# Kernel optimization log

Measured on AMD Instinct MI355X. Metric: run time of the kernel, lower is better.

## Reference

```python
import jax, jax.numpy as jnp
import numpy as np

EMBED_DIM = 1024
HEAD_DIM = 64
B, T = 4, 4096


def setup_inputs() -> dict:
    key = jax.random.key(0)
    kx, kq, kk, kv = jax.random.split(key, 4)
    x = jax.random.normal(kx, (B, T, EMBED_DIM), dtype=jnp.float32)
    # nn.Linear weights, stored transposed as (in, out) for x @ W
    s = 1.0 / np.sqrt(EMBED_DIM)
    Wq = jax.random.normal(kq, (EMBED_DIM, HEAD_DIM), dtype=jnp.float32) * s
    Wk = jax.random.normal(kk, (EMBED_DIM, HEAD_DIM), dtype=jnp.float32) * s
    Wv = jax.random.normal(kv, (EMBED_DIM, HEAD_DIM), dtype=jnp.float32) * s
    return {"x": x, "Wq": Wq, "Wk": Wk, "Wv": Wv}


def reference(x, Wq, Wk, Wv):
    Bc, Tc, C = x.shape
    Q = x @ Wq  # [B, T, H]
    K = x @ Wk
    V = x @ Wv
    # NOTE: original scales by embedding_dim C, not head_dim
    scores = jnp.einsum('bqh,bkh->bqk', Q, K) / jnp.sqrt(jnp.float32(C))
    causal = jnp.tril(jnp.ones((Tc, Tc), dtype=bool))
    scores = jnp.where(causal, scores, -jnp.inf)
    attn = jax.nn.softmax(scores, axis=-1)
    return jnp.einsum('bqk,bkh->bqh', attn, V)
```

## Files before the change

### kernel.cpp

```cpp
#include <hip/hip_runtime.h>
#include <hip/hip_bf16.h>
#include <math.h>

typedef __attribute__((ext_vector_type(8))) short bf16x8;
typedef __attribute__((ext_vector_type(4))) float f32x4;

#define MFMA16 __builtin_amdgcn_mfma_f32_16x16x32_bf16

static constexpr int TSEQ = 4096;
static constexpr int EMB = 1024;
static constexpr int HD = 64;

__device__ __forceinline__ unsigned short f2bf(float f) {
    unsigned u = __builtin_bit_cast(unsigned, f);
    u += 0x7fffu + ((u >> 16) & 1u);
    return (unsigned short)(u >> 16);
}
__device__ __forceinline__ int pk2bf(float a, float b) {
    return (int)((unsigned)f2bf(a) | ((unsigned)f2bf(b) << 16));
}

union frag_u { int i[4]; bf16x8 v; };

__global__ void prep_w(const float* __restrict__ Wq, const float* __restrict__ Wk,
                       const float* __restrict__ Wv, unsigned short* __restrict__ Wp) {
    int id = blockIdx.x * 256 + threadIdx.x;
    int wsel = id >> 16;
    int t = id & 65535;
    int k = t >> 6, n0 = t & 63;
    const float* W = (wsel == 0) ? Wq : (wsel == 1) ? Wk : Wv;
    float v = W[t];
    if (wsel == 0) v *= 0.03125f;
    int n = wsel * 64 + n0;
    Wp[(k >> 5) * 6144 + n * 32 + (k & 31)] = f2bf(v);
}

__global__ __launch_bounds__(256, 4) void proj_kernel(const float* __restrict__ X,
        const unsigned short* __restrict__ Wp, unsigned short* __restrict__ Qp,
        unsigned short* __restrict__ Kp, unsigned short* __restrict__ Vp) {
    const int lane = threadIdx.x & 63, wave = threadIdx.x >> 6;
    const int col = lane & 15, quad = lane >> 4;
    const int row0 = blockIdx.x * 16;

    f32x4 acc[3];
#pragma unroll
    for (int j = 0; j < 3; j++) acc[j] = (f32x4)(0.0f);

    const float* xr = X + (size_t)(row0 + col) * EMB + quad * 8;
    const char* wB = (const char*)Wp + wave * 1024 + col * 64 + quad * 16;

    float4 xa[3][2];
    bf16x8 wf[3][3];
#pragma unroll
    for (int p = 0; p < 3; p++) {
        const float* xp = xr + p * 32;
        xa[p][0] = *(const float4*)(xp);
        xa[p][1] = *(const float4*)(xp + 4);
        const char* wp = wB + (size_t)p * 12288;
#pragma unroll
        for (int j = 0; j < 3; j++) wf[p][j] = *(const bf16x8*)(wp + j * 4096);
    }

#pragma unroll
    for (int kc = 0; kc < 32; kc++) {
        const int s = kc % 3;
        frag_u A;
        A.i[0] = pk2bf(xa[s][0].x, xa[s][0].y);
        A.i[1] = pk2bf(xa[s][0].z, xa[s][0].w);
        A.i[2] = pk2bf(xa[s][1].x, xa[s][1].y);
        A.i[3] = pk2bf(xa[s][1].z, xa[s][1].w);
#pragma unroll
        for (int j = 0; j < 3; j++)
            acc[j] = MFMA16(A.v, wf[s][j], acc[j], 0, 0, 0);
        if (kc + 3 < 32) {
            const float* xp = xr + (kc + 3) * 32;
            xa[s][0] = *(const float4*)(xp);
            xa[s][1] = *(const float4*)(xp + 4);
            const char* wp = wB + (size_t)(kc + 3) * 12288;
#pragma unroll
            for (int j = 0; j < 3; j++) wf[s][j] = *(const bf16x8*)(wp + j * 4096);
        }
    }

    const int tile = blockIdx.x;
    const int c = tile >> 1, j2 = tile & 1;
#pragma unroll
    for (int r = 0; r < 4; r++)
        Qp[tile * 1024 + (wave >> 1) * 512 + (quad * 4 + r) * 32 +
           ((wave & 1) * 2 + (col >> 3)) * 8 + (col & 7)] = f2bf(acc[0][r]);
#pragma unroll
    for (int r = 0; r < 4; r++)
        Kp[(tile * 2 + (wave >> 1)) * 512 + (quad * 4 + r) * 32 +
           ((wave & 1) * 2 + (col >> 3)) * 8 + (col & 7)] = f2bf(acc[1][r]);
    {
        ushort4 pk;
        pk.x = f2bf(acc[2][0]); pk.y = f2bf(acc[2][1]);
        pk.z = f2bf(acc[2][2]); pk.w = f2bf(acc[2][3]);
        *(ushort4*)&Vp[c * 2048 + wave * 512 + col * 32 + j2 * 16 + quad * 4] = pk;
    }
}

__global__ __launch_bounds__(512, 4) void attn_kernel(const unsigned short* __restrict__ Qp,
        const unsigned short* __restrict__ Kp, const unsigned short* __restrict__ Vp,
        float* __restrict__ Out) {
    __shared__ float cmb[4][2][64][20];
    __shared__ unsigned short plds[8][2][640];
    const int lane = threadIdx.x & 63, wave = threadIdx.x >> 6;
    const int col = lane & 15, quad = lane >> 4;
    const int batch = blockIdx.x & 3;
    const int ti = 127 - (blockIdx.x >> 2);
    const int q0 = ti * 32;
    const size_t bT = (size_t)batch * TSEQ;
    const int fragoff = col * 64 + quad * 16;

    const char* QpB = (const char*)Qp;
    const char* KpB = (const char*)Kp;
    const char* VpB = (const char*)Vp;
    const int gt = (int)((bT + q0) >> 4);
    const int c0 = (int)(bT >> 5);

    bf16x8 aq[2][2];
#pragma unroll
    for (int m = 0; m < 2; m++)
#pragma unroll
        for (int h = 0; h < 2; h++)
            aq[m][h] = *(const bf16x8*)(QpB + (size_t)((gt + m) * 2 + h) * 1024 + fragoff);

    f32x4 o[2][4];
    f32x4 lsum[2];
#pragma unroll
    for (int m = 0; m < 2; m++) {
        lsum[m] = (f32x4)(0.0f);
#pragma unroll
        for (int t = 0; t < 4; t++) o[m][t] = (f32x4)(0.0f);
    }

    for (int c = wave; c <= ti; c += 8) {
        const char* kb = KpB + (size_t)(c0 + c) * 4096;
        const char* vb = VpB + (size_t)(c0 + c) * 4096;
        bf16x8 bk[2][2], bv[4];
#pragma unroll
        for (int j = 0; j < 2; j++)
#pragma unroll
            for (int h = 0; h < 2; h++)
                bk[j][h] = *(const bf16x8*)(kb + j * 2048 + h * 1024 + fragoff);
#pragma unroll
        for (int t = 0; t < 4; t++)
            bv[t] = *(const bf16x8*)(vb + t * 1024 + fragoff);

        f32x4 s[2][2];
#pragma unroll
        for (int m = 0; m < 2; m++)
#pragma unroll
            for (int j = 0; j < 2; j++) {
                f32x4 a = MFMA16(aq[m][0], bk[j][0], (f32x4)(0.0f), 0, 0, 0);
                s[m][j] = MFMA16(aq[m][1], bk[j][1], a, 0, 0, 0);
            }
        const bool diag = (c == ti);
#pragma unroll
        for (int m = 0; m < 2; m++)
#pragma unroll
            for (int j = 0; j < 2; j++)
#pragma unroll
                for (int r = 0; r < 4; r++) {
                    float v = s[m][j][r];
                    if (diag && (j * 16 + col > m * 16 + quad * 4 + r)) v = -INFINITY;
                    const float p = __expf(v);
                    lsum[m][r] += p;
                    plds[wave][m][(quad * 4 + r) * 40 + j * 16 + col] =
                        (unsigned short)(__builtin_bit_cast(unsigned, p) >> 16);
                }
        bf16x8 pa[2];
#pragma unroll
        for (int m = 0; m < 2; m++)
            pa[m] = *(const bf16x8*)(&plds[wave][m][col * 40 + quad * 8]);
#pragma unroll
        for (int m = 0; m < 2; m++)
#pragma unroll
            for (int t = 0; t < 4; t++)
                o[m][t] = MFMA16(pa[m], bv[t], o[m][t], 0, 0, 0);
    }

    auto wr = [&](int s) {
#pragma unroll
        for (int m = 0; m < 2; m++) {
#pragma unroll
            for (int t = 0; t < 4; t++)
                *(f32x4*)&cmb[s][m][lane][t * 4] = o[m][t];
            *(f32x4*)&cmb[s][m][lane][16] = lsum[m];
        }
    };
    auto rd = [&](int s) {
#pragma unroll
        for (int m = 0; m < 2; m++) {
#pragma unroll
            for (int t = 0; t < 4; t++)
                o[m][t] += *(const f32x4*)&cmb[s][m][lane][t * 4];
            lsum[m] += *(const f32x4*)&cmb[s][m][lane][16];
        }
    };
    if (wave >= 4) wr(wave - 4);
    __syncthreads();
    if (wave < 4) rd(wave);
    __syncthreads();
    if (wave == 2 || wave == 3) wr(wave);
    __syncthreads();
    if (wave < 2) rd(wave + 2);
    __syncthreads();
    if (wave == 1) wr(1);
    __syncthreads();
    if (wave == 0) {
        rd(1);
#pragma unroll
        for (int off = 1; off < 16; off <<= 1)
#pragma unroll
            for (int m = 0; m < 2; m++)
#pragma unroll
                for (int r = 0; r < 4; r++)
                    lsum[m][r] += __shfl_xor(lsum[m][r], off, 64);
#pragma unroll
        for (int m = 0; m < 2; m++)
#pragma unroll
            for (int r = 0; r < 4; r++) {
                const float inv = 1.0f / lsum[m][r];
                const size_t orow = (bT + q0 + m * 16 + quad * 4 + r) * HD;
#pragma unroll
                for (int t = 0; t < 4; t++)
                    Out[orow + t * 16 + col] = o[m][t][r] * inv;
            }
    }
}

extern "C" void kernel_launch(void* const* d_in, const int* in_sizes, int n_in,
                              void* d_out, int out_size, void* d_ws, size_t ws_size,
                              hipStream_t stream) {
    const float* x  = (const float*)d_in[0];
    const float* Wq = (const float*)d_in[1];
    const float* Wk = (const float*)d_in[2];
    const float* Wv = (const float*)d_in[3];
    float* out = (float*)d_out;

    char* w = (char*)d_ws;
    unsigned short* Wp = (unsigned short*)(w);
    unsigned short* Qp = (unsigned short*)(w + (512 << 10));
    unsigned short* Kp = (unsigned short*)(w + (512 << 10) + (2 << 20));
    unsigned short* Vp = (unsigned short*)(w + (512 << 10) + (4 << 20));

    hipLaunchKernelGGL(prep_w, dim3(768), dim3(256), 0, stream, Wq, Wk, Wv, Wp);
    hipLaunchKernelGGL(proj_kernel, dim3(1024), dim3(256), 0, stream, x, Wp, Qp, Kp, Vp);
    hipLaunchKernelGGL(attn_kernel, dim3(512), dim3(512), 0, stream, Qp, Kp, Vp, out);
}
```

Baseline: 166.7 us.

## Stage projection weights and X tiles through double-buffered LDS with warp specialization

The projection kernel now handles 32 rows per 512-thread block. Half the waves stream weight slabs into LDS via global_load_lds, and the other half convert X to bf16 into LDS, both double-buffered. All waves then read MFMA fragments from LDS, so each weight slab is fetched once per 32 rows instead of once per 16, halving weight traffic. The cost is a __syncthreads every k-step and serialized producer/consumer roles, which may limit latency hiding compared with the register prefetch it replaces.

New measurement: 147.2 us. 11.7% less time.

```diff
diff --git a/kernel.cpp b/kernel.cpp
--- a/kernel.cpp
+++ b/kernel.cpp
@@ -16,11 +16,12 @@
     u += 0x7fffu + ((u >> 16) & 1u);
     return (unsigned short)(u >> 16);
 }
-__device__ __forceinline__ int pk2bf(float a, float b) {
-    return (int)((unsigned)f2bf(a) | ((unsigned)f2bf(b) << 16));
-}
-
-union frag_u { int i[4]; bf16x8 v; };
+
+__device__ __forceinline__ void gll16(const void* g, void* l) {
+    __builtin_amdgcn_global_load_lds(
+        (const __attribute__((address_space(1))) void*)g,
+        (__attribute__((address_space(3))) void*)l, 16, 0, 0);
+}
 
 __global__ void prep_w(const float* __restrict__ Wq, const float* __restrict__ Wk,
                        const float* __restrict__ Wv, unsigned short* __restrict__ Wp) {
@@ -35,68 +36,83 @@
     Wp[(k >> 5) * 6144 + n * 32 + (k & 31)] = f2bf(v);
 }
 
-__global__ __launch_bounds__(256, 4) void proj_kernel(const float* __restrict__ X,
+__global__ __launch_bounds__(512, 4) void proj_kernel(const float* __restrict__ X,
         const unsigned short* __restrict__ Wp, unsigned short* __restrict__ Qp,
         unsigned short* __restrict__ Kp, unsigned short* __restrict__ Vp) {
-    const int lane = threadIdx.x & 63, wave = threadIdx.x >> 6;
+    __shared__ unsigned short wlds[2][6144];
+    __shared__ unsigned short xlds[2][1024];
+
+    const int tid = threadIdx.x;
+    const int lane = tid & 63, wave = tid >> 6;
     const int col = lane & 15, quad = lane >> 4;
-    const int row0 = blockIdx.x * 16;
+    const int mw = wave >> 2, nw = wave & 3;
+    const int row0 = blockIdx.x * 32;
 
     f32x4 acc[3];
 #pragma unroll
     for (int j = 0; j < 3; j++) acc[j] = (f32x4)(0.0f);
 
-    const float* xr = X + (size_t)(row0 + col) * EMB + quad * 8;
-    const char* wB = (const char*)Wp + wave * 1024 + col * 64 + quad * 16;
-
-    float4 xa[3][2];
-    bf16x8 wf[3][3];
-#pragma unroll
-    for (int p = 0; p < 3; p++) {
-        const float* xp = xr + p * 32;
-        xa[p][0] = *(const float4*)(xp);
-        xa[p][1] = *(const float4*)(xp + 4);
-        const char* wp = wB + (size_t)p * 12288;
-#pragma unroll
-        for (int j = 0; j < 3; j++) wf[p][j] = *(const bf16x8*)(wp + j * 4096);
-    }
-
-#pragma unroll
+    const char* wsrc = (const char*)Wp + lane * 16;
+    auto stageW = [&](int slab, int b) {
+        const char* s = wsrc + (size_t)slab * 12288;
+        char* d = (char*)&wlds[b][0];
+        gll16(s + nw * 1024,       d + nw * 1024);
+        gll16(s + (4 + nw) * 1024, d + (4 + nw) * 1024);
+        gll16(s + (8 + nw) * 1024, d + (8 + nw) * 1024);
+    };
+    const int u = tid - 256;
+    const int xrow = u >> 3, xseg = u & 7;
+    const float* xsrc = X + (size_t)(row0 + xrow) * EMB + xseg * 4;
+    const int xdst = (xrow >> 4) * 1024 + (xseg >> 1) * 256 + (xrow & 15) * 16 + (xseg & 1) * 8;
+
+    float4 xg = (float4)(0.0f);
+    if (mw == 1) {
+        float4 v = *(const float4*)(xsrc);
+        ushort4 p; p.x = f2bf(v.x); p.y = f2bf(v.y); p.z = f2bf(v.z); p.w = f2bf(v.w);
+        *(ushort4*)((char*)&xlds[0][0] + xdst) = p;
+        xg = *(const float4*)(xsrc + 32);
+    } else {
+        stageW(0, 0);
+    }
+    __syncthreads();
+
+#pragma unroll 2
     for (int kc = 0; kc < 32; kc++) {
-        const int s = kc % 3;
-        frag_u A;
-        A.i[0] = pk2bf(xa[s][0].x, xa[s][0].y);
-        A.i[1] = pk2bf(xa[s][0].z, xa[s][0].w);
-        A.i[2] = pk2bf(xa[s][1].x, xa[s][1].y);
-        A.i[3] = pk2bf(xa[s][1].z, xa[s][1].w);
-#pragma unroll
-        for (int j = 0; j < 3; j++)
-            acc[j] = MFMA16(A.v, wf[s][j], acc[j], 0, 0, 0);
-        if (kc + 3 < 32) {
-            const float* xp = xr + (kc + 3) * 32;
-            xa[s][0] = *(const float4*)(xp);
-            xa[s][1] = *(const float4*)(xp + 4);
-            const char* wp = wB + (size_t)(kc + 3) * 12288;
-#pragma unroll
-            for (int j = 0; j < 3; j++) wf[s][j] = *(const bf16x8*)(wp + j * 4096);
+        const int b = kc & 1;
+        if (mw == 0) {
+            if (kc + 1 < 32) stageW(kc + 1, b ^ 1);
+        } else {
+            if (kc + 1 < 32) {
+                float4 xn = xg;
+                if (kc + 2 < 32) xn = *(const float4*)(xsrc + (kc + 2) * 32);
+                ushort4 p; p.x = f2bf(xg.x); p.y = f2bf(xg.y);
+                p.z = f2bf(xg.z); p.w = f2bf(xg.w);
+                *(ushort4*)((char*)&xlds[b ^ 1][0] + xdst) = p;
+                xg = xn;
+            }
         }
-    }
-
-    const int tile = blockIdx.x;
-    const int c = tile >> 1, j2 = tile & 1;
+        const bf16x8 A = *(const bf16x8*)((const char*)&xlds[b][0] + mw * 1024 + lane * 16);
+        const char* wb = (const char*)&wlds[b][0] + col * 64 + quad * 16;
+        acc[0] = MFMA16(A, *(const bf16x8*)(wb + nw * 1024),       acc[0], 0, 0, 0);
+        acc[1] = MFMA16(A, *(const bf16x8*)(wb + (4 + nw) * 1024), acc[1], 0, 0, 0);
+        acc[2] = MFMA16(A, *(const bf16x8*)(wb + (8 + nw) * 1024), acc[2], 0, 0, 0);
+        __syncthreads();
+    }
+
+    const int tile = blockIdx.x * 2 + mw;
 #pragma unroll
     for (int r = 0; r < 4; r++)
-        Qp[tile * 1024 + (wave >> 1) * 512 + (quad * 4 + r) * 32 +
-           ((wave & 1) * 2 + (col >> 3)) * 8 + (col & 7)] = f2bf(acc[0][r]);
+        Qp[tile * 1024 + (nw >> 1) * 512 + (quad * 4 + r) * 32 +
+           ((nw & 1) * 2 + (col >> 3)) * 8 + (col & 7)] = f2bf(acc[0][r]);
 #pragma unroll
     for (int r = 0; r < 4; r++)
-        Kp[(tile * 2 + (wave >> 1)) * 512 + (quad * 4 + r) * 32 +
-           ((wave & 1) * 2 + (col >> 3)) * 8 + (col & 7)] = f2bf(acc[1][r]);
+        Kp[(tile * 2 + (nw >> 1)) * 512 + (quad * 4 + r) * 32 +
+           ((nw & 1) * 2 + (col >> 3)) * 8 + (col & 7)] = f2bf(acc[1][r]);
     {
         ushort4 pk;
         pk.x = f2bf(acc[2][0]); pk.y = f2bf(acc[2][1]);
         pk.z = f2bf(acc[2][2]); pk.w = f2bf(acc[2][3]);
-        *(ushort4*)&Vp[c * 2048 + wave * 512 + col * 32 + j2 * 16 + quad * 4] = pk;
+        *(ushort4*)&Vp[blockIdx.x * 2048 + nw * 512 + col * 32 + mw * 16 + quad * 4] = pk;
     }
 }
 
@@ -247,6 +263,6 @@
     unsigned short* Vp = (unsigned short*)(w + (512 << 10) + (4 << 20));
 
     hipLaunchKernelGGL(prep_w, dim3(768), dim3(256), 0, stream, Wq, Wk, Wv, Wp);
-    hipLaunchKernelGGL(proj_kernel, dim3(1024), dim3(256), 0, stream, x, Wp, Qp, Kp, Vp);
+    hipLaunchKernelGGL(proj_kernel, dim3(512), dim3(512), 0, stream, x, Wp, Qp, Kp, Vp);
     hipLaunchKernelGGL(attn_kernel, dim3(512), dim3(512), 0, stream, Qp, Kp, Vp, out);
 }
```
